# Kernel tuning notes

Measured on AMD Instinct MI355X. Metric: run time of the kernel, lower is better.

## Reference

```python
import jax, jax.numpy as jnp
import numpy as np
from jax.ops import segment_sum, segment_max

N_NODES = 50000
N_GRAPHS = 64
EPS = 1e-16


def gat_layer(x, src, dst, W, a_src, a_dst, b, n_nodes):
    # PyG GATConv, heads=1: shared linear, additive attention, per-dst softmax
    h = x @ W                                  # [N, H]
    al_s = h @ a_src                           # [N]
    al_d = h @ a_dst                           # [N]
    e = jax.nn.leaky_relu(al_s[src] + al_d[dst], 0.2)   # [E]
    # numerically stable segment softmax over edges grouped by dst
    m = segment_max(e, dst, num_segments=n_nodes)
    m = jnp.where(jnp.isfinite(m), m, 0.0)
    ex = jnp.exp(e - m[dst])
    denom = segment_sum(ex, dst, num_segments=n_nodes)
    alpha = ex / (denom[dst] + EPS)            # [E]
    out = segment_sum(alpha[:, None] * h[src], dst, num_segments=n_nodes)
    return out + b


def setup_inputs() -> dict:
    key = jax.random.key(0)
    ks = jax.random.split(key, 16)
    H = 128
    x = jax.random.normal(ks[0], (N_NODES, 4), dtype=jnp.float32)
    edge_index = jax.random.randint(ks[1], (2, 800000), 0, N_NODES, dtype=jnp.int64)
    batch = jnp.sort(jax.random.randint(ks[2], (N_NODES,), 0, N_GRAPHS, dtype=jnp.int64))

    def glorot(k, shape):
        lim = np.sqrt(6.0 / (shape[0] + shape[-1]))
        return jax.random.uniform(k, shape, jnp.float32, -lim, lim)

    params = {
        'W1': glorot(ks[3], (4, H)), 'as1': glorot(ks[4], (H,)), 'ad1': glorot(ks[5], (H,)), 'b1': jnp.zeros((H,), jnp.float32),
        'W2': glorot(ks[6], (H, H)), 'as2': glorot(ks[7], (H,)), 'ad2': glorot(ks[8], (H,)), 'b2': jnp.zeros((H,), jnp.float32),
        'W3': glorot(ks[9], (H, H)), 'as3': glorot(ks[10], (H,)), 'ad3': glorot(ks[11], (H,)), 'b3': jnp.zeros((H,), jnp.float32),
        'Wlin': glorot(ks[12], (H, 2)), 'blin': jnp.zeros((2,), jnp.float32),
    }
    return {'x': x, 'edge_index': edge_index, 'batch': batch, **params}


def reference(x, edge_index, batch, W1, as1, ad1, b1, W2, as2, ad2, b2, W3, as3, ad3, b3, Wlin, blin):
    n = x.shape[0]
    # GATConv default add_self_loops=True
    loop = jnp.arange(n, dtype=edge_index.dtype)
    src = jnp.concatenate([edge_index[0], loop])
    dst = jnp.concatenate([edge_index[1], loop])

    h = jax.nn.relu(gat_layer(x, src, dst, W1, as1, ad1, b1, n))
    h = jax.nn.relu(gat_layer(h, src, dst, W2, as2, ad2, b2, n))
    h = gat_layer(h, src, dst, W3, as3, ad3, b3, n)

    # global_mean_pool
    sums = segment_sum(h, batch, num_segments=N_GRAPHS)          # [G, H]
    cnt = segment_sum(jnp.ones((n,), h.dtype), batch, num_segments=N_GRAPHS)
    pooled = sums / jnp.maximum(cnt, 1.0)[:, None]
    # dropout p=0.5 is identity in eval mode
    return pooled @ Wlin + blin                                   # [G, 2]
```

## Files before the change

### kernel.cpp

```cpp
#include <hip/hip_runtime.h>
#include <math.h>


#define BW 512
#define PART_CHUNK 4096

typedef __attribute__((ext_vector_type(8))) short short8v;
typedef __attribute__((ext_vector_type(4))) float f32x4;

__device__ __forceinline__ float bflo(unsigned u) { return __uint_as_float(u << 16); }
__device__ __forceinline__ float bfhi(unsigned u) { return __uint_as_float(u & 0xffff0000u); }
__device__ __forceinline__ unsigned pk2bf(float a, float b) {
  unsigned ua = __float_as_uint(a); ua += 0x7fffu + ((ua >> 16) & 1u);
  unsigned ub = __float_as_uint(b); ub += 0x7fffu + ((ub >> 16) & 1u);
  return (ua >> 16) | (ub & 0xffff0000u);
}

__global__ __launch_bounds__(256) void kb_hist(const int* __restrict__ ei,
                                               int* __restrict__ bcnt,
                                               int E, int ET, int NB) {
  __shared__ int h[128];
  int tid = threadIdx.x;
  if (tid < 128) h[tid] = 0;
  __syncthreads();
  int stride = gridDim.x * 256;
  for (int i = blockIdx.x * 256 + tid; i < ET; i += stride) {
    int dst = (i < E) ? ei[E + i] : (i - E);
    atomicAdd(&h[dst >> 9], 1);
  }
  __syncthreads();
  if (tid < NB && h[tid] > 0) atomicAdd(&bcnt[tid], h[tid]);
}

__global__ __launch_bounds__(128) void kb_scan(const int* __restrict__ bcnt,
                                               int* __restrict__ bbase,
                                               int* __restrict__ bcur,
                                               int* __restrict__ rowp,
                                               int N, int ET, int NB) {
  __shared__ int sm[128];
  int t = threadIdx.x;
  int v = (t < NB) ? bcnt[t] : 0;
  sm[t] = v;
  __syncthreads();
  for (int off = 1; off < 128; off <<= 1) {
    int u = (t >= off) ? sm[t - off] : 0;
    __syncthreads();
    sm[t] += u;
    __syncthreads();
  }
  int pre = sm[t] - v;
  if (t <= NB) bbase[t] = pre;
  if (t < NB) bcur[t] = pre;
  if (t == 0) rowp[N] = ET;
}

__global__ __launch_bounds__(256) void kb_part(const int* __restrict__ ei,
                                               int* __restrict__ bcur,
                                               int* __restrict__ bucketed,
                                               int E, int ET, int NB) {
  __shared__ int hist[128];
  __shared__ int runb[128];
  int tid = threadIdx.x;
  int base = blockIdx.x * PART_CHUNK;
  if (tid < 128) hist[tid] = 0;

  int sv[16], dv[16];
#pragma unroll
  for (int k = 0; k < 16; ++k) {
    int j = base + k * 256 + tid;
    int s = -1, d = 0;
    if (j < ET) {
      if (j < E) { s = ei[j]; d = ei[E + j]; }
      else       { s = j - E; d = j - E; }
    }
    sv[k] = s; dv[k] = d;
  }
  __syncthreads();
#pragma unroll
  for (int k = 0; k < 16; ++k)
    if (sv[k] >= 0) atomicAdd(&hist[dv[k] >> 9], 1);
  __syncthreads();
  if (tid < NB && hist[tid] > 0) runb[tid] = atomicAdd(&bcur[tid], hist[tid]);
  __syncthreads();
  if (tid < 128) hist[tid] = 0;
  __syncthreads();
#pragma unroll
  for (int k = 0; k < 16; ++k) {
    if (sv[k] >= 0) {
      int b = dv[k] >> 9;
      int off = atomicAdd(&hist[b], 1);
      bucketed[runb[b] + off] = (sv[k] << 9) | (dv[k] & (BW - 1));
    }
  }
}

__global__ __launch_bounds__(256) void kb_csr(const int* __restrict__ bucketed,
                                              const int* __restrict__ bbase,
                                              int* __restrict__ rowp,
                                              int* __restrict__ csr,
                                              int N) {
  __shared__ int h[512];
  __shared__ int sm[256];
  __shared__ int cur[512];
  int tid = threadIdx.x;
  int b = blockIdx.x;
  int cb = bbase[b], ce = bbase[b + 1];

  h[tid] = 0; h[tid + 256] = 0;
  __syncthreads();
  for (int j = cb + tid; j < ce; j += 256)
    atomicAdd(&h[bucketed[j] & (BW - 1)], 1);
  __syncthreads();
  int a0 = h[2 * tid], a1 = h[2 * tid + 1];
  int s = a0 + a1;
  sm[tid] = s;
  __syncthreads();
  for (int off = 1; off < 256; off <<= 1) {
    int u = (tid >= off) ? sm[tid - off] : 0;
    __syncthreads();
    sm[tid] += u;
    __syncthreads();
  }
  int pre = sm[tid] - s;
  cur[2 * tid] = pre;
  cur[2 * tid + 1] = pre + a0;
  __syncthreads();
  int node0 = b * BW;
  for (int local = tid; local < BW; local += 256) {
    int node = node0 + local;
    if (node < N) rowp[node] = cb + cur[local];
  }
  __syncthreads();
  for (int j = cb + tid; j < ce; j += 256) {
    int p = bucketed[j];
    int loc = p & (BW - 1);
    int pos = cb + atomicAdd(&cur[loc], 1);
    csr[pos] = (unsigned)p >> 9;
  }
}

__global__ __launch_bounds__(256) void k_prep(const float* __restrict__ W2,
                                              const float* __restrict__ W3,
                                              const float* __restrict__ W1,
                                              const float* __restrict__ as1,
                                              const float* __restrict__ ad1,
                                              unsigned short* __restrict__ Wcm2,
                                              unsigned short* __restrict__ Wcm3,
                                              float* __restrict__ wv) {
  if (blockIdx.x == 64) {
    int lane = threadIdx.x;
    if (lane >= 64) return;
    float2 a = *(const float2*)(as1 + lane * 2);
    float2 d = *(const float2*)(ad1 + lane * 2);
    float ps[4], pd[4];
#pragma unroll
    for (int k = 0; k < 4; ++k) {
      float2 w = *(const float2*)(W1 + k * 128 + lane * 2);
      ps[k] = w.x * a.x + w.y * a.y;
      pd[k] = w.x * d.x + w.y * d.y;
    }
    for (int off = 32; off; off >>= 1) {
#pragma unroll
      for (int k = 0; k < 4; ++k) {
        ps[k] += __shfl_xor(ps[k], off);
        pd[k] += __shfl_xor(pd[k], off);
      }
    }
    if (lane == 0) {
#pragma unroll
      for (int k = 0; k < 4; ++k) { wv[k] = ps[k]; wv[4 + k] = pd[k]; }
    }
    return;
  }
  int i = blockIdx.x * 256 + threadIdx.x;
  if (i < 16384) {
    int k = i >> 7, n = i & 127;
    unsigned u = __float_as_uint(W2[i]); u += 0x7fffu + ((u >> 16) & 1u);
    Wcm2[n * 128 + k] = (unsigned short)(u >> 16);
    unsigned v = __float_as_uint(W3[i]); v += 0x7fffu + ((v >> 16) & 1u);
    Wcm3[n * 128 + k] = (unsigned short)(v >> 16);
  }
}

__global__ __launch_bounds__(256) void k_alnode(const float* __restrict__ X,
                                                const float* __restrict__ wv,
                                                float* __restrict__ al_s,
                                                float* __restrict__ al_d, int N) {
  int i = blockIdx.x * 256 + threadIdx.x;
  if (i >= N) return;
  float4 xv = *(const float4*)(X + i * 4);
  al_s[i] = xv.x * wv[0] + xv.y * wv[1] + xv.z * wv[2] + xv.w * wv[3];
  al_d[i] = xv.x * wv[4] + xv.y * wv[5] + xv.z * wv[6] + xv.w * wv[7];
}

__global__ __launch_bounds__(256) void k_aggx1(const int* __restrict__ csr_src,
                                               const int* __restrict__ rowp,
                                               const float* __restrict__ al_s,
                                               const float* __restrict__ al_d,
                                               const float* __restrict__ X,
                                               const float* __restrict__ W,
                                               const float* __restrict__ bias,
                                               float* __restrict__ exw,
                                               unsigned* __restrict__ Ybf, int N) {
  int wid = threadIdx.x >> 6, lane = threadIdx.x & 63;
  int dst = blockIdx.x * 4 + wid;
  if (dst >= N) return;
  int beg = rowp[dst], end = rowp[dst + 1];
  int deg = end - beg;
  float ald = al_d[dst];
  float4 acc = {0.f, 0.f, 0.f, 0.f};

  if (deg <= 64) {
    int srcv = 0;
    float e = -INFINITY;
    if (lane < deg) {
      srcv = csr_src[beg + lane];
      e = al_s[srcv] + ald;
      e = (e > 0.f) ? e : 0.2f * e;
    }
    float m = e;
    for (int off = 32; off; off >>= 1) m = fmaxf(m, __shfl_xor(m, off));
    float av = (lane < deg) ? __expf(e - m) : 0.f;
    float den = av;
    for (int off = 32; off; off >>= 1) den += __shfl_xor(den, off);
    av *= 1.0f / (den + 1e-16f);
    float4 xv = {0.f, 0.f, 0.f, 0.f};
    if (lane < deg) xv = *(const float4*)(X + (size_t)srcv * 4);
    acc.x = av * xv.x; acc.y = av * xv.y; acc.z = av * xv.z; acc.w = av * xv.w;
  } else {
    float m = -INFINITY;
    for (int j = beg + lane; j < end; j += 64) {
      float e = al_s[csr_src[j]] + ald;
      e = (e > 0.f) ? e : 0.2f * e;
      exw[j] = e;
      m = fmaxf(m, e);
    }
    for (int off = 32; off; off >>= 1) m = fmaxf(m, __shfl_xor(m, off));
    float den = 0.f;
    for (int j = beg + lane; j < end; j += 64) {
      float ex = __expf(exw[j] - m);
      exw[j] = ex;
      den += ex;
    }
    for (int off = 32; off; off >>= 1) den += __shfl_xor(den, off);
    float inv = 1.0f / (den + 1e-16f);
    for (int j = beg + lane; j < end; j += 64) {
      int s = csr_src[j];
      float w = exw[j] * inv;
      float4 xv = *(const float4*)(X + (size_t)s * 4);
      acc.x += w * xv.x; acc.y += w * xv.y; acc.z += w * xv.z; acc.w += w * xv.w;
    }
  }
  for (int off = 32; off; off >>= 1) {
    acc.x += __shfl_xor(acc.x, off);
    acc.y += __shfl_xor(acc.y, off);
    acc.z += __shfl_xor(acc.z, off);
    acc.w += __shfl_xor(acc.w, off);
  }
  int f = lane * 2;
  float2 w0 = *(const float2*)(W + f);
  float2 w1 = *(const float2*)(W + 128 + f);
  float2 w2 = *(const float2*)(W + 256 + f);
  float2 w3 = *(const float2*)(W + 384 + f);
  float2 bv = *(const float2*)(bias + f);
  float h0 = acc.x * w0.x + acc.y * w1.x + acc.z * w2.x + acc.w * w3.x + bv.x;
  float h1 = acc.x * w0.y + acc.y * w1.y + acc.z * w2.y + acc.w * w3.y + bv.y;
  h0 = fmaxf(h0, 0.f); h1 = fmaxf(h1, 0.f);
  Ybf[(size_t)dst * 64 + lane] = pk2bf(h0, h1);
}

__global__ __launch_bounds__(256) void k_gemm128mfma(
    const unsigned short* __restrict__ Xbf,
    const unsigned short* __restrict__ Wcm,
    const float* __restrict__ asv, const float* __restrict__ adv,
    unsigned* __restrict__ Hbf,
    float* __restrict__ al_s, float* __restrict__ al_d, int N) {
  int wid = threadIdx.x >> 6, lane = threadIdx.x & 63;
  int c = lane & 15, g = lane >> 4;
  int row0 = blockIdx.x * 64 + wid * 16;
  int arow = row0 + c;
  int arowc = (arow < N) ? arow : (N - 1);

  short8v a[4];
#pragma unroll
  for (int kt = 0; kt < 4; ++kt)
    a[kt] = *(const short8v*)(Xbf + (size_t)arowc * 128 + kt * 32 + g * 8);

  f32x4 acc[8];
#pragma unroll
  for (int f = 0; f < 8; ++f) acc[f] = (f32x4){0.f, 0.f, 0.f, 0.f};

#pragma unroll
  for (int f = 0; f < 8; ++f) {
    const unsigned short* wb = Wcm + (size_t)(f * 16 + c) * 128 + g * 8;
#pragma unroll
    for (int kt = 0; kt < 4; ++kt) {
      short8v b = *(const short8v*)(wb + kt * 32);
      acc[f] = __builtin_amdgcn_mfma_f32_16x16x32_bf16(a[kt], b, acc[f], 0, 0, 0);
    }
  }

  float ps[4] = {0.f, 0.f, 0.f, 0.f}, pd[4] = {0.f, 0.f, 0.f, 0.f};
#pragma unroll
  for (int f = 0; f < 8; ++f) {
    float as_c = asv[f * 16 + c], ad_c = adv[f * 16 + c];
#pragma unroll
    for (int j = 0; j < 4; ++j) { ps[j] += acc[f][j] * as_c; pd[j] += acc[f][j] * ad_c; }
  }
#pragma unroll
  for (int j = 0; j < 4; ++j) {
    for (int off = 1; off < 16; off <<= 1) {
      ps[j] += __shfl_xor(ps[j], off);
      pd[j] += __shfl_xor(pd[j], off);
    }
  }
  if (c == 0) {
#pragma unroll
    for (int j = 0; j < 4; ++j) {
      int r = row0 + g * 4 + j;
      if (r < N) { al_s[r] = ps[j]; al_d[r] = pd[j]; }
    }
  }

#pragma unroll
  for (int f = 0; f < 8; ++f) {
#pragma unroll
    for (int j = 0; j < 4; ++j) {
      float partner = __shfl_xor(acc[f][j], 1);
      int r = row0 + g * 4 + j;
      if (((lane & 1) == 0) && r < N)
        Hbf[(size_t)r * 64 + f * 8 + (c >> 1)] = pk2bf(acc[f][j], partner);
    }
  }
}

__global__ __launch_bounds__(256) void k_agg(const int* __restrict__ csr_src,
                                             const int* __restrict__ rowp,
                                             const float* __restrict__ al_s,
                                             const float* __restrict__ al_d,
                                             const uint4* __restrict__ Hbf,
                                             const float* __restrict__ bias,
                                             float* __restrict__ exw,
                                             uint4* __restrict__ Ybf,
                                             int N, int relu) {
  int wid = threadIdx.x >> 6, lane = threadIdx.x & 63;
  int dst = blockIdx.x * 4 + wid;
  if (dst >= N) return;
  int beg = rowp[dst], end = rowp[dst + 1];
  int deg = end - beg;
  float ald = al_d[dst];

  int q = lane >> 4;
  int l = lane & 15;
  float acc[8];
#pragma unroll
  for (int c = 0; c < 8; ++c) acc[c] = 0.f;

  if (deg <= 64) {
    int srcv = 0;
    float e = -INFINITY;
    if (lane < deg) {
      srcv = csr_src[beg + lane];
      e = al_s[srcv] + ald;
      e = (e > 0.f) ? e : 0.2f * e;
    }
    float m = e;
    for (int off = 32; off; off >>= 1) m = fmaxf(m, __shfl_xor(m, off));
    float av = (lane < deg) ? __expf(e - m) : 0.f;
    float den = av;
    for (int off = 32; off; off >>= 1) den += __shfl_xor(den, off);
    av *= 1.0f / (den + 1e-16f);

    int t = 0;
    for (; t + 16 <= deg; t += 16) {
      int s0 = __shfl(srcv, t + q);
      int s1 = __shfl(srcv, t + 4 + q);
      int s2 = __shfl(srcv, t + 8 + q);
      int s3 = __shfl(srcv, t + 12 + q);
      float w0 = __shfl(av, t + q);
      float w1 = __shfl(av, t + 4 + q);
      float w2 = __shfl(av, t + 8 + q);
      float w3 = __shfl(av, t + 12 + q);
      uint4 v0 = Hbf[(size_t)s0 * 16 + l];
      uint4 v1 = Hbf[(size_t)s1 * 16 + l];
      uint4 v2 = Hbf[(size_t)s2 * 16 + l];
      uint4 v3 = Hbf[(size_t)s3 * 16 + l];
      acc[0] += w0 * bflo(v0.x) + w1 * bflo(v1.x) + w2 * bflo(v2.x) + w3 * bflo(v3.x);
      acc[1] += w0 * bfhi(v0.x) + w1 * bfhi(v1.x) + w2 * bfhi(v2.x) + w3 * bfhi(v3.x);
      acc[2] += w0 * bflo(v0.y) + w1 * bflo(v1.y) + w2 * bflo(v2.y) + w3 * bflo(v3.y);
      acc[3] += w0 * bfhi(v0.y) + w1 * bfhi(v1.y) + w2 * bfhi(v2.y) + w3 * bfhi(v3.y);
      acc[4] += w0 * bflo(v0.z) + w1 * bflo(v1.z) + w2 * bflo(v2.z) + w3 * bflo(v3.z);
      acc[5] += w0 * bfhi(v0.z) + w1 * bfhi(v1.z) + w2 * bfhi(v2.z) + w3 * bfhi(v3.z);
      acc[6] += w0 * bflo(v0.w) + w1 * bflo(v1.w) + w2 * bflo(v2.w) + w3 * bflo(v3.w);
      acc[7] += w0 * bfhi(v0.w) + w1 * bfhi(v1.w) + w2 * bfhi(v2.w) + w3 * bfhi(v3.w);
    }
    if (t + 8 <= deg) {
      int sA = __shfl(srcv, t + q);
      int sB = __shfl(srcv, t + 4 + q);
      float wA = __shfl(av, t + q);
      float wB = __shfl(av, t + 4 + q);
      uint4 va = Hbf[(size_t)sA * 16 + l];
      uint4 vb = Hbf[(size_t)sB * 16 + l];
      acc[0] += wA * bflo(va.x) + wB * bflo(vb.x);
      acc[1] += wA * bfhi(va.x) + wB * bfhi(vb.x);
      acc[2] += wA * bflo(va.y) + wB * bflo(vb.y);
      acc[3] += wA * bfhi(va.y) + wB * bfhi(vb.y);
      acc[4] += wA * bflo(va.z) + wB * bflo(vb.z);
      acc[5] += wA * bfhi(va.z) + wB * bfhi(vb.z);
      acc[6] += wA * bflo(va.w) + wB * bflo(vb.w);
      acc[7] += wA * bfhi(va.w) + wB * bfhi(vb.w);
      t += 8;
    }
    if (t + 4 <= deg) {
      int sA = __shfl(srcv, t + q);
      float wA = __shfl(av, t + q);
      uint4 va = Hbf[(size_t)sA * 16 + l];
      acc[0] += wA * bflo(va.x); acc[1] += wA * bfhi(va.x);
      acc[2] += wA * bflo(va.y); acc[3] += wA * bfhi(va.y);
      acc[4] += wA * bflo(va.z); acc[5] += wA * bfhi(va.z);
      acc[6] += wA * bflo(va.w); acc[7] += wA * bfhi(va.w);
      t += 4;
    }
    {
      int sA = __shfl(srcv, t + q);
      float wA = __shfl(av, t + q);
      if (t + q < deg) {
        uint4 va = Hbf[(size_t)sA * 16 + l];
        acc[0] += wA * bflo(va.x); acc[1] += wA * bfhi(va.x);
        acc[2] += wA * bflo(va.y); acc[3] += wA * bfhi(va.y);
        acc[4] += wA * bflo(va.z); acc[5] += wA * bfhi(va.z);
        acc[6] += wA * bflo(va.w); acc[7] += wA * bfhi(va.w);
      }
    }
  } else {
    float m = -INFINITY;
    for (int j = beg + lane; j < end; j += 64) {
      float e = al_s[csr_src[j]] + ald;
      e = (e > 0.f) ? e : 0.2f * e;
      exw[j] = e;
      m = fmaxf(m, e);
    }
    for (int off = 32; off; off >>= 1) m = fmaxf(m, __shfl_xor(m, off));

    float den = 0.f;
    for (int j = beg + lane; j < end; j += 64) {
      float ex = __expf(exw[j] - m);
      exw[j] = ex;
      den += ex;
    }
    for (int off = 32; off; off >>= 1) den += __shfl_xor(den, off);
    float inv = 1.0f / (den + 1e-16f);

    for (int j = beg + q; j < end; j += 4) {
      int sA = csr_src[j];
      float wA = exw[j] * inv;
      uint4 va = Hbf[(size_t)sA * 16 + l];
      acc[0] += wA * bflo(va.x); acc[1] += wA * bfhi(va.x);
      acc[2] += wA * bflo(va.y); acc[3] += wA * bfhi(va.y);
      acc[4] += wA * bflo(va.z); acc[5] += wA * bfhi(va.z);
      acc[6] += wA * bflo(va.w); acc[7] += wA * bfhi(va.w);
    }
  }

#pragma unroll
  for (int c = 0; c < 8; ++c) {
    acc[c] += __shfl_xor(acc[c], 16);
    acc[c] += __shfl_xor(acc[c], 32);
  }
  if (q == 0) {
    float4 bv0 = *(const float4*)(bias + l * 8);
    float4 bv1 = *(const float4*)(bias + l * 8 + 4);
    float o0 = acc[0] + bv0.x, o1 = acc[1] + bv0.y, o2 = acc[2] + bv0.z, o3 = acc[3] + bv0.w;
    float o4 = acc[4] + bv1.x, o5 = acc[5] + bv1.y, o6 = acc[6] + bv1.z, o7 = acc[7] + bv1.w;
    if (relu) {
      o0 = fmaxf(o0, 0.f); o1 = fmaxf(o1, 0.f); o2 = fmaxf(o2, 0.f); o3 = fmaxf(o3, 0.f);
      o4 = fmaxf(o4, 0.f); o5 = fmaxf(o5, 0.f); o6 = fmaxf(o6, 0.f); o7 = fmaxf(o7, 0.f);
    }
    uint4 pb;
    pb.x = pk2bf(o0, o1); pb.y = pk2bf(o2, o3);
    pb.z = pk2bf(o4, o5); pb.w = pk2bf(o6, o7);
    Ybf[(size_t)dst * 16 + l] = pb;
  }
}

__global__ __launch_bounds__(256) void k_pool(const unsigned* __restrict__ Ybf,
                                              const int* __restrict__ batch,
                                              float* __restrict__ gsum,
                                              float* __restrict__ gcnt,
                                              int N, int nwaves) {
  int gw = (blockIdx.x * 256 + threadIdx.x) >> 6;
  int lane = threadIdx.x & 63;
  int chunk = (N + nwaves - 1) / nwaves;
  int beg = gw * chunk;
  int end = beg + chunk; if (end > N) end = N;
  if (beg >= end) return;

  int curg = batch[beg];
  float2 acc = {0.f, 0.f};
  int cnt = 0;
  for (int n = beg; n < end; ++n) {
    int g = batch[n];
    if (g != curg) {
      atomicAdd(&gsum[curg * 128 + lane * 2], acc.x);
      atomicAdd(&gsum[curg * 128 + lane * 2 + 1], acc.y);
      if (lane == 0) atomicAdd(&gcnt[curg], (float)cnt);
      acc.x = 0.f; acc.y = 0.f; cnt = 0; curg = g;
    }
    unsigned u = Ybf[(size_t)n * 64 + lane];
    acc.x += bflo(u); acc.y += bfhi(u);
    ++cnt;
  }
  atomicAdd(&gsum[curg * 128 + lane * 2], acc.x);
  atomicAdd(&gsum[curg * 128 + lane * 2 + 1], acc.y);
  if (lane == 0) atomicAdd(&gcnt[curg], (float)cnt);
}

__global__ __launch_bounds__(128) void k_final(const float* __restrict__ gsum,
                                               const float* __restrict__ gcnt,
                                               const float* __restrict__ Wlin,
                                               const float* __restrict__ blin,
                                               float* __restrict__ out) {
  int t = threadIdx.x;
  int g = t >> 1, c = t & 1;
  float inv = 1.0f / fmaxf(gcnt[g], 1.0f);
  float acc = blin[c];
  for (int k = 0; k < 128; ++k) acc += gsum[g * 128 + k] * inv * Wlin[k * 2 + c];
  out[g * 2 + c] = acc;
}

extern "C" void kernel_launch(void* const* d_in, const int* in_sizes, int n_in,
                              void* d_out, int out_size, void* d_ws, size_t ws_size,
                              hipStream_t stream) {
  const float* x    = (const float*)d_in[0];
  const int*   ei   = (const int*)d_in[1];
  const int*   batch= (const int*)d_in[2];
  const float* W1   = (const float*)d_in[3];
  const float* as1  = (const float*)d_in[4];
  const float* ad1  = (const float*)d_in[5];
  const float* b1   = (const float*)d_in[6];
  const float* W2   = (const float*)d_in[7];
  const float* as2  = (const float*)d_in[8];
  const float* ad2  = (const float*)d_in[9];
  const float* b2   = (const float*)d_in[10];
  const float* W3   = (const float*)d_in[11];
  const float* as3  = (const float*)d_in[12];
  const float* ad3  = (const float*)d_in[13];
  const float* b3   = (const float*)d_in[14];
  const float* Wlin = (const float*)d_in[15];
  const float* blin = (const float*)d_in[16];

  int N = in_sizes[0] / 4;
  int E = in_sizes[1] / 2;
  int ET = E + N;
  int NB = (N + BW - 1) / BW;

  char* ws = (char*)d_ws;
  unsigned* bfA = (unsigned*)ws; ws += (size_t)N * 64 * 4;
  unsigned* bfB = (unsigned*)ws; ws += (size_t)N * 64 * 4;
  float* al_s = (float*)ws; ws += (size_t)N * 4;
  float* al_d = (float*)ws; ws += (size_t)N * 4;
  float* wv   = (float*)ws; ws += (size_t)64 * 4;
  float* gsum = (float*)ws; ws += (size_t)64 * 128 * 4;
  float* gcnt = (float*)ws; ws += (size_t)64 * 4;
  int* rowp   = (int*)ws;   ws += (size_t)(N + 1) * 4;
  int* csr    = (int*)ws;   ws += (size_t)ET * 4;
  float* exw  = (float*)ws; ws += (size_t)ET * 4;
  int* bucketed = (int*)ws; ws += (size_t)ET * 4;
  int* bcnt   = (int*)ws;   ws += (size_t)128 * 4;
  int* bbase  = (int*)ws;   ws += (size_t)132 * 4;
  int* bcur   = (int*)ws;   ws += (size_t)128 * 4;
  unsigned short* wcm2 = (unsigned short*)ws; ws += (size_t)128 * 128 * 2;
  unsigned short* wcm3 = (unsigned short*)ws; ws += (size_t)128 * 128 * 2;

  hipMemsetAsync(bcnt, 0, (size_t)128 * 4, stream);
  hipMemsetAsync(gsum, 0, (size_t)(64 * 128 + 64) * 4, stream);

  kb_hist<<<256, 256, 0, stream>>>(ei, bcnt, E, ET, NB);
  kb_scan<<<1, 128, 0, stream>>>(bcnt, bbase, bcur, rowp, N, ET, NB);
  kb_part<<<(ET + PART_CHUNK - 1) / PART_CHUNK, 256, 0, stream>>>(ei, bcur, bucketed, E, ET, NB);
  kb_csr <<<NB, 256, 0, stream>>>(bucketed, bbase, rowp, csr, N);
  k_prep <<<65, 256, 0, stream>>>(W2, W3, W1, as1, ad1, wcm2, wcm3, wv);

  int nb4 = (N + 3) / 4;
  int nb64 = (N + 63) / 64;
  k_alnode<<<(N + 255) / 256, 256, 0, stream>>>(x, wv, al_s, al_d, N);
  k_aggx1 <<<nb4, 256, 0, stream>>>(csr, rowp, al_s, al_d, x, W1, b1, exw, bfB, N);
  k_gemm128mfma<<<nb64, 256, 0, stream>>>((const unsigned short*)bfB, wcm2, as2, ad2, bfA, al_s, al_d, N);
  k_agg        <<<nb4, 256, 0, stream>>>(csr, rowp, al_s, al_d, (const uint4*)bfA, b2, exw, (uint4*)bfB, N, 1);
  k_gemm128mfma<<<nb64, 256, 0, stream>>>((const unsigned short*)bfB, wcm3, as3, ad3, bfA, al_s, al_d, N);
  k_agg        <<<nb4, 256, 0, stream>>>(csr, rowp, al_s, al_d, (const uint4*)bfA, b3, exw, (uint4*)bfB, N, 0);

  k_pool <<<256, 256, 0, stream>>>(bfB, batch, gsum, gcnt, N, 1024);
  k_final<<<1, 128, 0, stream>>>(gsum, gcnt, Wlin, blin, (float*)d_out);
}
```

Baseline: 317.7 us.

## Drop memsets and alnode kernel, use per-block histograms and nontemporal stores

Removes the two hipMemsetAsync calls. The histogram kernel now writes per-block partial counts that the scan kernel reduces, so bcnt no longer needs zeroing, and gsum is zeroed by extra blocks in k_prep. The k_alnode kernel is removed: layer-1 attention logits are computed inline in k_aggx1 from the gathered x rows. Bf16 activation stores in the aggregation and GEMM kernels become nontemporal. The scan now reads 256x128 partials serially per thread, and nontemporal stores may hurt if the next kernel would have hit those writes in cache.

```diff
diff --git a/kernel.cpp b/kernel.cpp
--- a/kernel.cpp
+++ b/kernel.cpp
@@ -4,9 +4,11 @@
 
 #define BW 512
 #define PART_CHUNK 4096
+#define HIST_WGS 256
 
 typedef __attribute__((ext_vector_type(8))) short short8v;
 typedef __attribute__((ext_vector_type(4))) float f32x4;
+typedef __attribute__((ext_vector_type(4))) unsigned uint4v;
 
 __device__ __forceinline__ float bflo(unsigned u) { return __uint_as_float(u << 16); }
 __device__ __forceinline__ float bfhi(unsigned u) { return __uint_as_float(u & 0xffff0000u); }
@@ -17,29 +19,31 @@
 }
 
 __global__ __launch_bounds__(256) void kb_hist(const int* __restrict__ ei,
-                                               int* __restrict__ bcnt,
-                                               int E, int ET, int NB) {
+                                               int* __restrict__ bpart,
+                                               int E, int ET) {
   __shared__ int h[128];
   int tid = threadIdx.x;
   if (tid < 128) h[tid] = 0;
   __syncthreads();
-  int stride = gridDim.x * 256;
+  int stride = HIST_WGS * 256;
   for (int i = blockIdx.x * 256 + tid; i < ET; i += stride) {
     int dst = (i < E) ? ei[E + i] : (i - E);
     atomicAdd(&h[dst >> 9], 1);
   }
   __syncthreads();
-  if (tid < NB && h[tid] > 0) atomicAdd(&bcnt[tid], h[tid]);
-}
-
-__global__ __launch_bounds__(128) void kb_scan(const int* __restrict__ bcnt,
+  if (tid < 128) bpart[blockIdx.x * 128 + tid] = h[tid];
+}
+
+__global__ __launch_bounds__(128) void kb_scan(const int* __restrict__ bpart,
                                                int* __restrict__ bbase,
                                                int* __restrict__ bcur,
                                                int* __restrict__ rowp,
                                                int N, int ET, int NB) {
   __shared__ int sm[128];
   int t = threadIdx.x;
-  int v = (t < NB) ? bcnt[t] : 0;
+  int v = 0;
+  for (int w = 0; w < HIST_WGS; ++w) v += bpart[w * 128 + t];
+  if (t >= NB) v = 0;
   sm[t] = v;
   __syncthreads();
   for (int off = 1; off < 128; off <<= 1) {
@@ -146,7 +150,13 @@
                                               const float* __restrict__ ad1,
                                               unsigned short* __restrict__ Wcm2,
                                               unsigned short* __restrict__ Wcm3,
-                                              float* __restrict__ wv) {
+                                              float* __restrict__ wv,
+                                              float* __restrict__ gsum) {
+  if (blockIdx.x >= 65) {
+    int idx = (blockIdx.x - 65) * 256 + threadIdx.x;
+    if (idx < 64 * 128 + 64) gsum[idx] = 0.f;
+    return;
+  }
   if (blockIdx.x == 64) {
     int lane = threadIdx.x;
     if (lane >= 64) return;
@@ -182,21 +192,9 @@
   }
 }
 
-__global__ __launch_bounds__(256) void k_alnode(const float* __restrict__ X,
-                                                const float* __restrict__ wv,
-                                                float* __restrict__ al_s,
-                                                float* __restrict__ al_d, int N) {
-  int i = blockIdx.x * 256 + threadIdx.x;
-  if (i >= N) return;
-  float4 xv = *(const float4*)(X + i * 4);
-  al_s[i] = xv.x * wv[0] + xv.y * wv[1] + xv.z * wv[2] + xv.w * wv[3];
-  al_d[i] = xv.x * wv[4] + xv.y * wv[5] + xv.z * wv[6] + xv.w * wv[7];
-}
-
 __global__ __launch_bounds__(256) void k_aggx1(const int* __restrict__ csr_src,
                                                const int* __restrict__ rowp,
-                                               const float* __restrict__ al_s,
-                                               const float* __restrict__ al_d,
+                                               const float* __restrict__ wv,
                                                const float* __restrict__ X,
                                                const float* __restrict__ W,
                                                const float* __restrict__ bias,
@@ -207,15 +205,20 @@
   if (dst >= N) return;
   int beg = rowp[dst], end = rowp[dst + 1];
   int deg = end - beg;
-  float ald = al_d[dst];
+  float wvs0 = wv[0], wvs1 = wv[1], wvs2 = wv[2], wvs3 = wv[3];
+  float4 xd = *(const float4*)(X + (size_t)dst * 4);
+  float ald = xd.x * wv[4] + xd.y * wv[5] + xd.z * wv[6] + xd.w * wv[7];
   float4 acc = {0.f, 0.f, 0.f, 0.f};
 
   if (deg <= 64) {
     int srcv = 0;
     float e = -INFINITY;
+    float4 xv = {0.f, 0.f, 0.f, 0.f};
     if (lane < deg) {
       srcv = csr_src[beg + lane];
-      e = al_s[srcv] + ald;
+      xv = *(const float4*)(X + (size_t)srcv * 4);
+      float als = xv.x * wvs0 + xv.y * wvs1 + xv.z * wvs2 + xv.w * wvs3;
+      e = als + ald;
       e = (e > 0.f) ? e : 0.2f * e;
     }
     float m = e;
@@ -224,13 +227,13 @@
     float den = av;
     for (int off = 32; off; off >>= 1) den += __shfl_xor(den, off);
     av *= 1.0f / (den + 1e-16f);
-    float4 xv = {0.f, 0.f, 0.f, 0.f};
-    if (lane < deg) xv = *(const float4*)(X + (size_t)srcv * 4);
     acc.x = av * xv.x; acc.y = av * xv.y; acc.z = av * xv.z; acc.w = av * xv.w;
   } else {
     float m = -INFINITY;
     for (int j = beg + lane; j < end; j += 64) {
-      float e = al_s[csr_src[j]] + ald;
+      int s = csr_src[j];
+      float4 xv = *(const float4*)(X + (size_t)s * 4);
+      float e = xv.x * wvs0 + xv.y * wvs1 + xv.z * wvs2 + xv.w * wvs3 + ald;
       e = (e > 0.f) ? e : 0.2f * e;
       exw[j] = e;
       m = fmaxf(m, e);
@@ -266,7 +269,7 @@
   float h0 = acc.x * w0.x + acc.y * w1.x + acc.z * w2.x + acc.w * w3.x + bv.x;
   float h1 = acc.x * w0.y + acc.y * w1.y + acc.z * w2.y + acc.w * w3.y + bv.y;
   h0 = fmaxf(h0, 0.f); h1 = fmaxf(h1, 0.f);
-  Ybf[(size_t)dst * 64 + lane] = pk2bf(h0, h1);
+  __builtin_nontemporal_store(pk2bf(h0, h1), Ybf + (size_t)dst * 64 + lane);
 }
 
 __global__ __launch_bounds__(256) void k_gemm128mfma(
@@ -329,7 +332,8 @@
       float partner = __shfl_xor(acc[f][j], 1);
       int r = row0 + g * 4 + j;
       if (((lane & 1) == 0) && r < N)
-        Hbf[(size_t)r * 64 + f * 8 + (c >> 1)] = pk2bf(acc[f][j], partner);
+        __builtin_nontemporal_store(pk2bf(acc[f][j], partner),
+                                    Hbf + (size_t)r * 64 + f * 8 + (c >> 1));
     }
   }
 }
@@ -341,7 +345,7 @@
                                              const uint4* __restrict__ Hbf,
                                              const float* __restrict__ bias,
                                              float* __restrict__ exw,
-                                             uint4* __restrict__ Ybf,
+                                             unsigned* __restrict__ Ybf,
                                              int N, int relu) {
   int wid = threadIdx.x >> 6, lane = threadIdx.x & 63;
   int dst = blockIdx.x * 4 + wid;
@@ -476,10 +480,10 @@
       o0 = fmaxf(o0, 0.f); o1 = fmaxf(o1, 0.f); o2 = fmaxf(o2, 0.f); o3 = fmaxf(o3, 0.f);
       o4 = fmaxf(o4, 0.f); o5 = fmaxf(o5, 0.f); o6 = fmaxf(o6, 0.f); o7 = fmaxf(o7, 0.f);
     }
-    uint4 pb;
+    uint4v pb;
     pb.x = pk2bf(o0, o1); pb.y = pk2bf(o2, o3);
     pb.z = pk2bf(o4, o5); pb.w = pk2bf(o6, o7);
-    Ybf[(size_t)dst * 16 + l] = pb;
+    __builtin_nontemporal_store(pb, (uint4v*)(Ybf + (size_t)dst * 64 + l * 4));
   }
 }
 
@@ -566,29 +570,25 @@
   int* csr    = (int*)ws;   ws += (size_t)ET * 4;
   float* exw  = (float*)ws; ws += (size_t)ET * 4;
   int* bucketed = (int*)ws; ws += (size_t)ET * 4;
-  int* bcnt   = (int*)ws;   ws += (size_t)128 * 4;
+  int* bpart  = (int*)ws;   ws += (size_t)HIST_WGS * 128 * 4;
   int* bbase  = (int*)ws;   ws += (size_t)132 * 4;
   int* bcur   = (int*)ws;   ws += (size_t)128 * 4;
   unsigned short* wcm2 = (unsigned short*)ws; ws += (size_t)128 * 128 * 2;
   unsigned short* wcm3 = (unsigned short*)ws; ws += (size_t)128 * 128 * 2;
 
-  hipMemsetAsync(bcnt, 0, (size_t)128 * 4, stream);
-  hipMemsetAsync(gsum, 0, (size_t)(64 * 128 + 64) * 4, stream);
-
-  kb_hist<<<256, 256, 0, stream>>>(ei, bcnt, E, ET, NB);
-  kb_scan<<<1, 128, 0, stream>>>(bcnt, bbase, bcur, rowp, N, ET, NB);
+  kb_hist<<<HIST_WGS, 256, 0, stream>>>(ei, bpart, E, ET);
+  kb_scan<<<1, 128, 0, stream>>>(bpart, bbase, bcur, rowp, N, ET, NB);
   kb_part<<<(ET + PART_CHUNK - 1) / PART_CHUNK, 256, 0, stream>>>(ei, bcur, bucketed, E, ET, NB);
   kb_csr <<<NB, 256, 0, stream>>>(bucketed, bbase, rowp, csr, N);
-  k_prep <<<65, 256, 0, stream>>>(W2, W3, W1, as1, ad1, wcm2, wcm3, wv);
+  k_prep <<<98, 256, 0, stream>>>(W2, W3, W1, as1, ad1, wcm2, wcm3, wv, gsum);
 
   int nb4 = (N + 3) / 4;
   int nb64 = (N + 63) / 64;
-  k_alnode<<<(N + 255) / 256, 256, 0, stream>>>(x, wv, al_s, al_d, N);
-  k_aggx1 <<<nb4, 256, 0, stream>>>(csr, rowp, al_s, al_d, x, W1, b1, exw, bfB, N);
+  k_aggx1<<<nb4, 256, 0, stream>>>(csr, rowp, wv, x, W1, b1, exw, bfB, N);
   k_gemm128mfma<<<nb64, 256, 0, stream>>>((const unsigned short*)bfB, wcm2, as2, ad2, bfA, al_s, al_d, N);
-  k_agg        <<<nb4, 256, 0, stream>>>(csr, rowp, al_s, al_d, (const uint4*)bfA, b2, exw, (uint4*)bfB, N, 1);
+  k_agg        <<<nb4, 256, 0, stream>>>(csr, rowp, al_s, al_d, (const uint4*)bfA, b2, exw, bfB, N, 1);
   k_gemm128mfma<<<nb64, 256, 0, stream>>>((const unsigned short*)bfB, wcm3, as3, ad3, bfA, al_s, al_d, N);
-  k_agg        <<<nb4, 256, 0, stream>>>(csr, rowp, al_s, al_d, (const uint4*)bfA, b3, exw, (uint4*)bfB, N, 0);
+  k_agg        <<<nb4, 256, 0, stream>>>(csr, rowp, al_s, al_d, (const uint4*)bfA, b3, exw, bfB, N, 0);
 
   k_pool <<<256, 256, 0, stream>>>(bfB, batch, gsum, gcnt, N, 1024);
   k_final<<<1, 128, 0, stream>>>(gsum, gcnt, Wlin, blin, (float*)d_out);
```

Result: no change. 312.5 us (-1.6%).
